# Kernel optimization log

Measured on AMD Instinct MI355X. Metric: run time of the kernel, lower is better.

Reference implementation:

```python
import jax, jax.numpy as jnp
import numpy as np

B, T, D, F0, F1 = 128, 256, 512, 2048, 1024
EPS = 1e-5  # BatchNorm1d eps


def _bn_relu(x, gamma, beta):
    # training-mode BatchNorm1d over the flattened (B*T) batch axis, then ReLU
    mu = x.mean(axis=0)
    var = x.var(axis=0)  # biased variance, as torch BN uses for normalization
    return jax.nn.relu((x - mu) * jax.lax.rsqrt(var + EPS) * gamma + beta)


def _lstm_cell(x, h, c, w_ih, w_hh, b):
    # torch LSTMCell gate order: i, f, g, o
    gates = x @ w_ih.T + h @ w_hh.T + b
    i, f, g, o = jnp.split(gates, 4, axis=-1)
    c = jax.nn.sigmoid(f) * c + jax.nn.sigmoid(i) * jnp.tanh(g)
    h = jax.nn.sigmoid(o) * jnp.tanh(c)
    return h, c


def setup_inputs() -> dict:
    key = jax.random.key(0)
    ks = jax.random.split(key, 24)
    s = 0.02
    inp = {
        "feat0": jax.random.normal(ks[0], (B, T, F0), jnp.float32),
        "feat1": jax.random.normal(ks[1], (B, T, F1), jnp.float32),
        "feat_mask": jnp.ones((B, T), jnp.float32),
        # visual embeddings (Linear + BN affine)
        "w_emb0": jax.random.normal(ks[2], (D, F0), jnp.float32) * s,
        "b_emb0": jnp.zeros((D,), jnp.float32),
        "gamma0": jnp.ones((D,), jnp.float32),
        "beta0": jnp.zeros((D,), jnp.float32),
        "w_emb1": jax.random.normal(ks[3], (D, F1), jnp.float32) * s,
        "b_emb1": jnp.zeros((D,), jnp.float32),
        "gamma1": jnp.ones((D,), jnp.float32),
        "beta1": jnp.zeros((D,), jnp.float32),
        # LSTMCell rgb
        "w_ih0": jax.random.normal(ks[4], (4 * D, D), jnp.float32) * s,
        "w_hh0": jax.random.normal(ks[5], (4 * D, D), jnp.float32) * s,
        "b_ih0": jnp.zeros((4 * D,), jnp.float32),
        "b_hh0": jnp.zeros((4 * D,), jnp.float32),
        # LSTMCell opfl
        "w_ih1": jax.random.normal(ks[6], (4 * D, D), jnp.float32) * s,
        "w_hh1": jax.random.normal(ks[7], (4 * D, D), jnp.float32) * s,
        "b_ih1": jnp.zeros((4 * D,), jnp.float32),
        "b_hh1": jnp.zeros((4 * D,), jnp.float32),
        # Gates: sigmoid(Linear(source)) * target
        "wg0": jax.random.normal(ks[8], (D, D), jnp.float32) * s,
        "bg0": jnp.zeros((D,), jnp.float32),
        "wg1": jax.random.normal(ks[9], (D, D), jnp.float32) * s,
        "bg1": jnp.zeros((D,), jnp.float32),
        # Fusion: tanh(W1 f1 + W2 f2 + b)
        "wf1": jax.random.normal(ks[10], (D, D), jnp.float32) * s,
        "wf2": jax.random.normal(ks[11], (D, D), jnp.float32) * s,
        "bf": jnp.zeros((D,), jnp.float32),
    }
    return inp


def reference(feat0, feat1, feat_mask,
              w_emb0, b_emb0, gamma0, beta0,
              w_emb1, b_emb1, gamma1, beta1,
              w_ih0, w_hh0, b_ih0, b_hh0,
              w_ih1, w_hh1, b_ih1, b_hh1,
              wg0, bg0, wg1, bg1,
              wf1, wf2, bf):
    Bv, Tv = feat0.shape[0], feat0.shape[1]
    # embed + BN(train mode) + ReLU (dropout = identity in eval)
    e0 = _bn_relu(feat0.reshape(-1, feat0.shape[-1]) @ w_emb0.T + b_emb0,
                  gamma0, beta0).reshape(Bv, Tv, -1)
    e1 = _bn_relu(feat1.reshape(-1, feat1.shape[-1]) @ w_emb1.T + b_emb1,
                  gamma1, beta1).reshape(Bv, Tv, -1)

    bc0 = b_ih0 + b_hh0
    bc1 = b_ih1 + b_hh1

    def step(carry, xs):
        h0, c0, h1, c1 = carry
        x0, x1, m = xs  # x: [B, D], m: [B]
        h0, c0 = _lstm_cell(x0, h0, c0, w_ih0, w_hh0, bc0)
        h1, c1 = _lstm_cell(x1, h1, c1, w_ih1, w_hh1, bc1)
        m = m[:, None]
        h0, c0, h1, c1 = h0 * m, c0 * m, h1 * m, c1 * m
        gate0 = jax.nn.sigmoid(h1 @ wg0.T + bg0) * h0  # gate_rgb(h1 -> h0)
        gate1 = jax.nn.sigmoid(h0 @ wg1.T + bg1) * h1  # gate_opfl(h0 -> h1)
        return (h0, c0, h1, c1), (gate0, gate1)

    z = jnp.zeros((Bv, w_hh0.shape[-1]), e0.dtype)
    xs = (e0.transpose(1, 0, 2), e1.transpose(1, 0, 2), feat_mask.T)
    _, (o0, o1) = jax.lax.scan(step, (z, z, z, z), xs)  # [T, B, D]
    o0 = o0.transpose(1, 0, 2)
    o1 = o1.transpose(1, 0, 2)
    # Fusion: tanh(W1 o0 + W2 o1 + b)
    return jnp.tanh(jnp.einsum('btd,ed->bte', o0, wf1)
                    + jnp.einsum('btd,ed->bte', o1, wf2) + bf)
```

## Files before the change

kernel.cpp:

```cpp
#include <hip/hip_runtime.h>
#include <math.h>


typedef short s16x8 __attribute__((ext_vector_type(8)));
typedef float f32x4 __attribute__((ext_vector_type(4)));
typedef float f32x16 __attribute__((ext_vector_type(16)));
typedef unsigned short u16;

__device__ __forceinline__ float sigmoidf_(float x){ return 1.0f/(1.0f+expf(-x)); }

__device__ __forceinline__ u16 f2bf(float x){
  unsigned int u = __float_as_uint(x);
  unsigned int r = u + 0x7fffu + ((u>>16)&1u);
  return (u16)(r>>16);
}
__device__ __forceinline__ float bf2f(u16 s){ return __uint_as_float(((unsigned int)s)<<16); }

__device__ __forceinline__ void unpack8(const unsigned int* __restrict__ p,
                                        s16x8& hi, s16x8& lo){
  uint4 w0 = *(const uint4*)p;
  uint4 w1 = *(const uint4*)(p+4);
  union { unsigned int u[4]; s16x8 v; } H, L;
  H.u[0] = (w0.x>>16) | (w0.y & 0xffff0000u);
  H.u[1] = (w0.z>>16) | (w0.w & 0xffff0000u);
  H.u[2] = (w1.x>>16) | (w1.y & 0xffff0000u);
  H.u[3] = (w1.z>>16) | (w1.w & 0xffff0000u);
  L.u[0] = (w0.x & 0xffffu) | (w0.y<<16);
  L.u[1] = (w0.z & 0xffffu) | (w0.w<<16);
  L.u[2] = (w1.x & 0xffffu) | (w1.y<<16);
  L.u[3] = (w1.z & 0xffffu) | (w1.w<<16);
  hi = H.v; lo = L.v;
}

__global__ __launch_bounds__(256) void split_plain(const float* __restrict__ src,
                                                   u16* __restrict__ hi, u16* __restrict__ lo, int n)
{
  int i = blockIdx.x*256 + threadIdx.x;
  if (i < n){
    float v = src[i];
    u16 h = f2bf(v);
    hi[i] = h;
    lo[i] = f2bf(v - bf2f(h));
  }
}

__global__ __launch_bounds__(256) void split_fragW(const float* __restrict__ src,
                                                   u16* __restrict__ hi, u16* __restrict__ lo,
                                                   int N, int K)
{
  int i = blockIdx.x*256 + threadIdx.x;
  if (i >= N*K) return;
  int n = i / K, k = i - n*K;
  float v = src[i];
  u16 h = f2bf(v), l2 = f2bf(v - bf2f(h));
  size_t off = ((((size_t)(k>>4)*(N/32) + (n>>5))*64) + ((k>>3)&1)*32 + (n&31))*8 + (k&7);
  hi[off] = h; lo[off] = l2;
}

__global__ __launch_bounds__(256) void split_gates2(const float* __restrict__ wih,
                                                    const float* __restrict__ whh,
                                                    const float* __restrict__ bih,
                                                    const float* __restrict__ bhh,
                                                    u16* __restrict__ hi, u16* __restrict__ lo,
                                                    float* __restrict__ bc)
{
  int np = blockIdx.x;
  int d = np>>2, q = np&3;
  int orow = q*512 + d;
  for (int k = threadIdx.x; k < 1024; k += 256){
    float v = (k < 512) ? wih[(size_t)orow*512 + k] : whh[(size_t)orow*512 + (k-512)];
    u16 h = f2bf(v), l2 = f2bf(v - bf2f(h));
    size_t off = (((size_t)(k>>4)*64 + (np>>5))*64 + ((k>>3)&1)*32 + (np&31))*8 + (k&7);
    hi[off] = h; lo[off] = l2;
  }
  if (threadIdx.x == 0) bc[np] = bih[orow] + bhh[orow];
}

__global__ __launch_bounds__(256) void gemm_emb(
    const float* __restrict__ A, const u16* __restrict__ Whi, const u16* __restrict__ Wlo,
    const float* __restrict__ bias, float* __restrict__ out, int K)
{
  __shared__ u16 Ah[128][40];
  __shared__ u16 Al[128][40];
  __shared__ u16 Wh[128][40];
  __shared__ u16 Wl[128][40];

  int bx = blockIdx.x;
  int nt = bx & 3, mt = bx >> 2;
  int m0 = mt*128, n0 = nt*128;
  int tid = threadIdx.x, lane = tid & 63, w = tid >> 6;
  int wm = (w>>1)*64, wn = (w&1)*64;

  f32x4 acc[4][4];
  #pragma unroll
  for (int i=0;i<4;i++)
    #pragma unroll
    for (int j=0;j<4;j++) acc[i][j] = (f32x4){0.f,0.f,0.f,0.f};

  for (int k0=0; k0<K; k0+=32){
    #pragma unroll
    for (int p=0;p<4;p++){
      int fi = p*256 + tid;
      int r = fi>>3, c = fi&7;
      float4 v = *(const float4*)&A[(size_t)(m0+r)*K + k0 + c*4];
      u16 h0=f2bf(v.x), h1=f2bf(v.y), h2=f2bf(v.z), h3=f2bf(v.w);
      u16 l0=f2bf(v.x-bf2f(h0)), l1=f2bf(v.y-bf2f(h1)), l2=f2bf(v.z-bf2f(h2)), l3=f2bf(v.w-bf2f(h3));
      uint2 ph = { (unsigned)h0 | ((unsigned)h1<<16), (unsigned)h2 | ((unsigned)h3<<16) };
      uint2 pl = { (unsigned)l0 | ((unsigned)l1<<16), (unsigned)l2 | ((unsigned)l3<<16) };
      *(uint2*)&Ah[r][c*4] = ph;
      *(uint2*)&Al[r][c*4] = pl;
    }
    #pragma unroll
    for (int p=0;p<2;p++){
      int fi = p*256 + tid;
      int r = fi>>2, c = fi&3;
      uint4 vh = *(const uint4*)&Whi[(size_t)(n0+r)*K + k0 + c*8];
      uint4 vl = *(const uint4*)&Wlo[(size_t)(n0+r)*K + k0 + c*8];
      *(uint4*)&Wh[r][c*8] = vh;
      *(uint4*)&Wl[r][c*8] = vl;
    }
    __syncthreads();
    s16x8 ah[4], al[4];
    #pragma unroll
    for (int mf=0;mf<4;mf++){
      ah[mf] = *(const s16x8*)&Ah[wm + mf*16 + (lane&15)][(lane>>4)*8];
      al[mf] = *(const s16x8*)&Al[wm + mf*16 + (lane&15)][(lane>>4)*8];
    }
    #pragma unroll
    for (int nf=0;nf<4;nf++){
      s16x8 wh = *(const s16x8*)&Wh[wn + nf*16 + (lane&15)][(lane>>4)*8];
      s16x8 wl = *(const s16x8*)&Wl[wn + nf*16 + (lane&15)][(lane>>4)*8];
      #pragma unroll
      for (int mf=0;mf<4;mf++){
        acc[mf][nf] = __builtin_amdgcn_mfma_f32_16x16x32_bf16(ah[mf], wh, acc[mf][nf], 0,0,0);
        acc[mf][nf] = __builtin_amdgcn_mfma_f32_16x16x32_bf16(ah[mf], wl, acc[mf][nf], 0,0,0);
        acc[mf][nf] = __builtin_amdgcn_mfma_f32_16x16x32_bf16(al[mf], wh, acc[mf][nf], 0,0,0);
      }
    }
    __syncthreads();
  }
  #pragma unroll
  for (int mf=0;mf<4;mf++){
    #pragma unroll
    for (int nf=0;nf<4;nf++){
      int col = n0 + wn + nf*16 + (lane&15);
      int row0 = m0 + wm + mf*16 + (lane>>4)*4;
      float b = bias[col];
      #pragma unroll
      for (int g=0; g<4; ++g){
        out[(size_t)(row0+g)*512 + col] = acc[mf][nf][g] + b;
      }
    }
  }
}

__global__ __launch_bounds__(256) void bn_stats1(const float* __restrict__ Y,
                                                 float* __restrict__ psum,
                                                 float* __restrict__ psq)
{
  int blk = blockIdx.x;
  int tid = threadIdx.x;
  const float* base = Y + (size_t)blk*256*512;
  float sx=0.f, sy=0.f, qx=0.f, qy=0.f;
  for (int r=0;r<256;r++){
    float2 v = *(const float2*)&base[(size_t)r*512 + tid*2];
    sx += v.x; sy += v.y; qx += v.x*v.x; qy += v.y*v.y;
  }
  psum[(size_t)blk*512 + tid*2]   = sx;
  psum[(size_t)blk*512 + tid*2+1] = sy;
  psq [(size_t)blk*512 + tid*2]   = qx;
  psq [(size_t)blk*512 + tid*2+1] = qy;
}

__global__ __launch_bounds__(512) void bn_stats2(const float* __restrict__ psum,
                                                 const float* __restrict__ psq,
                                                 float* __restrict__ mean,
                                                 float* __restrict__ scale)
{
  int c = threadIdx.x;
  float s=0.f, q=0.f;
  for (int b=0;b<128;b++){ s += psum[(size_t)b*512+c]; q += psq[(size_t)b*512+c]; }
  float mu = s * (1.0f/32768.0f);
  float var = q * (1.0f/32768.0f) - mu*mu;
  mean[c] = mu;
  scale[c] = rsqrtf(var + 1e-5f);
}

__global__ __launch_bounds__(256) void bn_apply_split(const float* __restrict__ Y,
                                                      const float* __restrict__ mean,
                                                      const float* __restrict__ scale,
                                                      const float* __restrict__ gamma,
                                                      const float* __restrict__ beta,
                                                      u16* __restrict__ ehi, u16* __restrict__ elo)
{
  size_t idx = (size_t)blockIdx.x*256 + threadIdx.x;
  int r = (int)(idx >> 6);
  int c0 = (int)(idx & 63) * 8;
  int b = r >> 8, t = r & 255;
  float4 v0 = *(const float4*)&Y[(size_t)r*512 + c0];
  float4 v1 = *(const float4*)&Y[(size_t)r*512 + c0 + 4];
  float vv[8] = {v0.x,v0.y,v0.z,v0.w,v1.x,v1.y,v1.z,v1.w};
  unsigned int hw[4], lw[4];
  #pragma unroll
  for (int u=0;u<8;u+=2){
    float xa = fmaxf((vv[u]  -mean[c0+u])  *scale[c0+u]  *gamma[c0+u]  +beta[c0+u],   0.f);
    float xb = fmaxf((vv[u+1]-mean[c0+u+1])*scale[c0+u+1]*gamma[c0+u+1]+beta[c0+u+1], 0.f);
    u16 ha = f2bf(xa), hb = f2bf(xb);
    u16 la = f2bf(xa - bf2f(ha)), lb = f2bf(xb - bf2f(hb));
    hw[u>>1] = (unsigned)ha | ((unsigned)hb<<16);
    lw[u>>1] = (unsigned)la | ((unsigned)lb<<16);
  }
  size_t off = (size_t)t*65536 + ((((size_t)(c0>>4)*4 + (b>>5))*64) + ((c0>>3)&1)*32 + (b&31))*8;
  uint4 ph = {hw[0],hw[1],hw[2],hw[3]};
  uint4 pl = {lw[0],lw[1],lw[2],lw[3]};
  *(uint4*)&ehi[off] = ph;
  *(uint4*)&elo[off] = pl;
}

__global__ __launch_bounds__(256) void zero_init(int* __restrict__ bar,
                                                 unsigned* __restrict__ H0,
                                                 unsigned* __restrict__ H1)
{
  int i = blockIdx.x*256 + threadIdx.x;
  if (i < 6144) bar[i] = 0;
  H0[i] = 0u;
  H1[i] = 0u;
}

struct ScanArgs {
  const u16 *e0hi, *e0lo, *e1hi, *e1lo;
  const u16 *wr0hi, *wr0lo, *wr1hi, *wr1lo;
  const float *bc0, *bc1, *mask;
  unsigned *H0, *H1;
  int *flags;
  int *gen;
};

__global__ __launch_bounds__(256) void scan_all(ScanArgs A)
{
  __shared__ u16 Wlds[64][64][8];
  __shared__ float red[2][2][16][65];
  __shared__ int sig;
  __shared__ int fcnt;

  int bx = blockIdx.x;
  int ci = bx>>7, s = (bx>>1)&63, rh = bx&1;
  int dom = ci*2 + rh;
  int cb = s;
  int tid = threadIdx.x, lane = tid&63, w = tid>>6;
  int khalf = w>>1, pr = w&1;
  int rt = rh*2 + pr;
  bool mast = (cb == 0);

  int* flags = A.flags + dom*64*16;
  int* gen   = A.gen   + dom*32*16;

  const u16* ehi = ci? A.e1hi : A.e0hi;
  const u16* elo = ci? A.e1lo : A.e0lo;
  const u16* whi = ci? A.wr1hi : A.wr0hi;
  const u16* wlo = ci? A.wr1lo : A.wr0lo;
  const float* bc = ci? A.bc1 : A.bc0;
  unsigned* Hc = ci? A.H1 : A.H0;

  if (tid == 0){ sig = 0; fcnt = 0; }

  for (int it=0; it<16; ++it){
    int cid = it*256 + tid;
    int ks = cid>>6, l8 = cid&63;
    const u16* src = whi + (((size_t)ks*64 + s)*64 + l8)*8;
    *(uint4*)&Wlds[ks][l8][0] = *(const uint4*)src;
  }
  __syncthreads();

  int q = lane&3;
  int np = s*32 + (lane&31);
  int d  = np>>2;
  float bcv = bc[np];
  float creg[4] = {0.f,0.f,0.f,0.f};

  for (int t=0; t<256; ++t){
    size_t abase = (size_t)t*65536;

    if (khalf == 0){
      f32x16 a0=(f32x16)(0.f), a1=(f32x16)(0.f), a2=(f32x16)(0.f);
      #pragma unroll 4
      for (int kk=0; kk<32; ++kk){
        size_t aoff = abase + ((size_t)(kk*4 + rt)*64 + lane)*8;
        s16x8 fah = *(const s16x8*)(ehi + aoff);
        s16x8 fal = *(const s16x8*)(elo + aoff);
        s16x8 fwh = *(const s16x8*)&Wlds[kk][lane][0];
        s16x8 fwl = *(const s16x8*)(wlo + (((size_t)kk*64 + s)*64 + lane)*8);
        a0 = __builtin_amdgcn_mfma_f32_32x32x16_bf16(fah, fwh, a0, 0,0,0);
        a1 = __builtin_amdgcn_mfma_f32_32x32x16_bf16(fah, fwl, a1, 0,0,0);
        a2 = __builtin_amdgcn_mfma_f32_32x32x16_bf16(fal, fwh, a2, 0,0,0);
      }
      f32x16 t3 = a0 + a1 + a2;
      #pragma unroll
      for (int e=0;e<16;e++) red[t&1][pr][e][lane] = t3[e];
      __syncthreads();
    } else {
      if (lane == 0){
        while (__hip_atomic_load(&gen[(cb&31)*16], __ATOMIC_RELAXED, __HIP_MEMORY_SCOPE_AGENT) < t)
          __builtin_amdgcn_s_sleep(1);
      }
      asm volatile("" ::: "memory");

      f32x16 a0=(f32x16)(0.f), a1=(f32x16)(0.f), a2=(f32x16)(0.f);
      #pragma unroll 8
      for (int kk=0; kk<32; ++kk){
        size_t aoff = abase + ((size_t)(kk*4 + rt)*64 + lane)*8;
        s16x8 fah, fal;
        unpack8(Hc + aoff, fah, fal);
        int ks = 32 + kk;
        s16x8 fwh = *(const s16x8*)&Wlds[ks][lane][0];
        s16x8 fwl = *(const s16x8*)(wlo + (((size_t)ks*64 + s)*64 + lane)*8);
        a0 = __builtin_amdgcn_mfma_f32_32x32x16_bf16(fah, fwh, a0, 0,0,0);
        a1 = __builtin_amdgcn_mfma_f32_32x32x16_bf16(fah, fwl, a1, 0,0,0);
        a2 = __builtin_amdgcn_mfma_f32_32x32x16_bf16(fal, fwh, a2, 0,0,0);
      }
      f32x16 mine = a0 + a1 + a2;
      __syncthreads();

      f32x16 tot;
      #pragma unroll
      for (int e=0;e<16;e++) tot[e] = mine[e] + red[t&1][pr][e][lane];

      size_t hSlot = (size_t)(t+1)*65536;
      #pragma unroll
      for (int r=0;r<16;r++){
        float pre = tot[r] + bcv;
        float act = (q==2) ? tanhf(pre) : sigmoidf_(pre);
        float v1 = __shfl_xor(act, 1);
        float v2 = __shfl_xor(act, 2);
        float v3 = __shfl_xor(v1, 2);
        float gi = (q==0)? act : (q==1)? v1 : (q==2)? v2 : v3;
        float gf = (q==1)? act : (q==0)? v1 : (q==3)? v2 : v3;
        float gg = (q==2)? act : (q==3)? v1 : (q==0)? v2 : v3;
        float go = (q==3)? act : (q==2)? v1 : (q==1)? v2 : v3;
        if (q == (r&3)){
          int ri = r>>2;
          int row = rh*64 + pr*32 + (r&3) + 8*ri + 4*(lane>>5);
          float cold = creg[ri];
          float cn = gf*cold + gi*gg;
          float h  = go*tanhf(cn);
          float mv = A.mask[(size_t)row*256 + t];
          cn *= mv; h *= mv;
          creg[ri] = cn;
          u16 hh = f2bf(h), hl = f2bf(h - bf2f(hh));
          size_t hoff = hSlot + ((((size_t)(d>>4)*4 + (row>>5))*64) + ((d>>3)&1)*32 + (row&31))*8 + (d&7);
          atomicExch(&Hc[hoff], ((unsigned)hh<<16) | (unsigned)hl);
        }
      }
      asm volatile("s_waitcnt vmcnt(0)" ::: "memory");
      if (lane == 0) atomicAdd(&sig, 1);

      if (mast){
        int fi = tid - 128;
        if (fi >= 1 && fi < 64){
          while (__hip_atomic_load(&flags[fi*16], __ATOMIC_RELAXED, __HIP_MEMORY_SCOPE_AGENT) < t+1)
            __builtin_amdgcn_s_sleep(1);
          atomicAdd(&fcnt, 1);
        }
        if (tid == 128){
          while (__hip_atomic_load(&sig, __ATOMIC_RELAXED, __HIP_MEMORY_SCOPE_WORKGROUP) < 2*(t+1))
            __builtin_amdgcn_s_sleep(1);
          while (__hip_atomic_load(&fcnt, __ATOMIC_RELAXED, __HIP_MEMORY_SCOPE_WORKGROUP) < 63*(t+1))
            __builtin_amdgcn_s_sleep(1);
        }
        if (w == 2 && lane < 32){
          atomicExch(&gen[lane*16], t+1);
        }
      } else {
        if (tid == 128){
          while (__hip_atomic_load(&sig, __ATOMIC_RELAXED, __HIP_MEMORY_SCOPE_WORKGROUP) < 2*(t+1))
            __builtin_amdgcn_s_sleep(1);
          atomicExch(&flags[cb*16], t+1);
        }
      }
    }
  }
}

__global__ __launch_bounds__(256,1) void gemm_gate(
    const unsigned* __restrict__ Aint,
    const u16* __restrict__ Whi,  const u16* __restrict__ Wlo,
    const float* __restrict__ bias,
    const unsigned* __restrict__ OtInt,
    u16* __restrict__ outHi, u16* __restrict__ outLo)
{
  int bx = blockIdx.x;
  int nt = bx & 7, mt = bx >> 3;
  int n0 = nt*64;
  int tid = threadIdx.x, lane = tid & 63, w = tid >> 6;
  size_t aBase = (size_t)mt*65536;

  f32x16 a0[2], a1[2], a2[2];
  #pragma unroll
  for (int c=0;c<2;c++){
    a0[c]=(f32x16)(0.f); a1[c]=(f32x16)(0.f); a2[c]=(f32x16)(0.f);
  }

  #pragma unroll 2
  for (int kk=0; kk<32; ++kk){
    size_t aoff = aBase + (((size_t)kk*4 + w)*64 + lane)*8;
    s16x8 fah, fal;
    unpack8(Aint + aoff, fah, fal);
    #pragma unroll
    for (int c=0;c<2;c++){
      size_t woff = (((size_t)kk*16 + nt*2 + c)*64 + lane)*8;
      s16x8 fwh = *(const s16x8*)(Whi + woff);
      s16x8 fwl = *(const s16x8*)(Wlo + woff);
      a0[c] = __builtin_amdgcn_mfma_f32_32x32x16_bf16(fah, fwh, a0[c], 0,0,0);
      a1[c] = __builtin_amdgcn_mfma_f32_32x32x16_bf16(fah, fwl, a1[c], 0,0,0);
      a2[c] = __builtin_amdgcn_mfma_f32_32x32x16_bf16(fal, fwh, a2[c], 0,0,0);
    }
  }

  #pragma unroll
  for (int c=0;c<2;c++){
    f32x16 acc = a0[c] + a1[c] + a2[c];
    int col = n0 + c*32 + (lane&31);
    float b = bias[col];
    #pragma unroll
    for (int r=0;r<16;r++){
      int row = w*32 + (r&3) + 8*(r>>2) + 4*(lane>>5);
      float v = acc[r] + b;
      size_t foff = aBase + ((((size_t)(col>>4)*4 + w)*64) + ((col>>3)&1)*32 + (row&31))*8 + (col&7);
      unsigned ov = OtInt[foff];
      float other = bf2f((u16)(ov>>16)) + bf2f((u16)(ov&0xffffu));
      v = sigmoidf_(v) * other;
      u16 hh = f2bf(v);
      u16 hl = f2bf(v - bf2f(hh));
      outHi[foff] = hh;
      outLo[foff] = hl;
    }
  }
}

__global__ __launch_bounds__(256,1) void gemm_final(
    const u16* __restrict__ Ahi,  const u16* __restrict__ Alo,
    const u16* __restrict__ A2hi, const u16* __restrict__ A2lo,
    const u16* __restrict__ Whi,  const u16* __restrict__ Wlo,
    const u16* __restrict__ W2hi, const u16* __restrict__ W2lo,
    const float* __restrict__ bias,
    float* __restrict__ outF)
{
  int bx = blockIdx.x;
  int nt = bx & 7, mt = bx >> 3;
  int n0 = nt*64;
  int tid = threadIdx.x, lane = tid & 63, w = tid >> 6;
  size_t aBase = (size_t)mt*65536;

  f32x16 a0[2], a1[2], a2[2];
  #pragma unroll
  for (int c=0;c<2;c++){
    a0[c]=(f32x16)(0.f); a1[c]=(f32x16)(0.f); a2[c]=(f32x16)(0.f);
  }

  for (int pair=0; pair<2; ++pair){
    const u16* ah = pair ? A2hi : Ahi;
    const u16* al = pair ? A2lo : Alo;
    const u16* wh = pair ? W2hi : Whi;
    const u16* wl = pair ? W2lo : Wlo;
    #pragma unroll 2
    for (int kk=0; kk<32; ++kk){
      size_t aoff = aBase + (((size_t)kk*4 + w)*64 + lane)*8;
      s16x8 fah = *(const s16x8*)(ah + aoff);
      s16x8 fal = *(const s16x8*)(al + aoff);
      #pragma unroll
      for (int c=0;c<2;c++){
        size_t woff = (((size_t)kk*16 + nt*2 + c)*64 + lane)*8;
        s16x8 fwh = *(const s16x8*)(wh + woff);
        s16x8 fwl = *(const s16x8*)(wl + woff);
        a0[c] = __builtin_amdgcn_mfma_f32_32x32x16_bf16(fah, fwh, a0[c], 0,0,0);
        a1[c] = __builtin_amdgcn_mfma_f32_32x32x16_bf16(fah, fwl, a1[c], 0,0,0);
        a2[c] = __builtin_amdgcn_mfma_f32_32x32x16_bf16(fal, fwh, a2[c], 0,0,0);
      }
    }
  }

  #pragma unroll
  for (int c=0;c<2;c++){
    f32x16 acc = a0[c] + a1[c] + a2[c];
    int col = n0 + c*32 + (lane&31);
    float b = bias[col];
    #pragma unroll
    for (int r=0;r<16;r++){
      int row = w*32 + (r&3) + 8*(r>>2) + 4*(lane>>5);
      float v = tanhf(acc[r] + b);
      outF[((size_t)row*256 + mt)*512 + col] = v;
    }
  }
}

extern "C" void kernel_launch(void* const* d_in, const int* in_sizes, int n_in,
                              void* d_out, int out_size, void* d_ws, size_t ws_size,
                              hipStream_t stream)
{
  const float* feat0  = (const float*)d_in[0];
  const float* feat1  = (const float*)d_in[1];
  const float* fmask  = (const float*)d_in[2];
  const float* w_emb0 = (const float*)d_in[3];
  const float* b_emb0 = (const float*)d_in[4];
  const float* gamma0 = (const float*)d_in[5];
  const float* beta0  = (const float*)d_in[6];
  const float* w_emb1 = (const float*)d_in[7];
  const float* b_emb1 = (const float*)d_in[8];
  const float* gamma1 = (const float*)d_in[9];
  const float* beta1  = (const float*)d_in[10];
  const float* w_ih0  = (const float*)d_in[11];
  const float* w_hh0  = (const float*)d_in[12];
  const float* b_ih0  = (const float*)d_in[13];
  const float* b_hh0  = (const float*)d_in[14];
  const float* w_ih1  = (const float*)d_in[15];
  const float* w_hh1  = (const float*)d_in[16];
  const float* b_ih1  = (const float*)d_in[17];
  const float* b_hh1  = (const float*)d_in[18];
  const float* wg0    = (const float*)d_in[19];
  const float* bg0    = (const float*)d_in[20];
  const float* wg1    = (const float*)d_in[21];
  const float* bg1    = (const float*)d_in[22];
  const float* wf1    = (const float*)d_in[23];
  const float* wf2    = (const float*)d_in[24];
  const float* bf     = (const float*)d_in[25];
  float* out = (float*)d_out;

  char* ws = (char*)d_ws;
  u16* e0hi = (u16*)(ws + 0);
  u16* e0lo = (u16*)(ws + 33554432);
  u16* e1hi = (u16*)(ws + 67108864);
  u16* e1lo = (u16*)(ws + 100663296);
  unsigned* H0int = (unsigned*)(ws + 134217728);
  unsigned* H1int = (unsigned*)(ws + 201588736);
  int*   barp  = (int*)(ws + 269484032);
  float* psum  = (float*)(ws + 269484032);
  float* psq   = (float*)(ws + 269746176);
  float* meanb = (float*)(ws + 270008320);
  float* scaleb= (float*)(ws + 270010368);
  float* bc0   = (float*)(ws + 270012416);
  float* bc1   = (float*)(ws + 270020608);
  u16* wr0hi = (u16*)(ws + 270028800);
  u16* wr0lo = (u16*)(ws + 274223104);
  u16* wr1hi = (u16*)(ws + 278417408);
  u16* wr1lo = (u16*)(ws + 282611712);
  u16* we0hi = (u16*)(ws + 286806016);
  u16* we0lo = (u16*)(ws + 288903168);
  u16* we1hi = (u16*)(ws + 291000320);
  u16* we1lo = (u16*)(ws + 292048896);
  u16* wg0hi = (u16*)(ws + 293097472);
  u16* wg0lo = (u16*)(ws + 293621760);
  u16* wg1hi = (u16*)(ws + 294146048);
  u16* wg1lo = (u16*)(ws + 294670336);
  u16* wf1hi = (u16*)(ws + 295194624);
  u16* wf1lo = (u16*)(ws + 295718912);
  u16* wf2hi = (u16*)(ws + 296243200);
  u16* wf2lo = (u16*)(ws + 296767488);
  float* Ytmp = (float*)(ws + 134217728);

  split_gates2<<<dim3(2048), dim3(256), 0, stream>>>(w_ih0, w_hh0, b_ih0, b_hh0, wr0hi, wr0lo, bc0);
  split_gates2<<<dim3(2048), dim3(256), 0, stream>>>(w_ih1, w_hh1, b_ih1, b_hh1, wr1hi, wr1lo, bc1);
  split_plain<<<dim3(4096), dim3(256), 0, stream>>>(w_emb0, we0hi, we0lo, 1048576);
  split_plain<<<dim3(2048), dim3(256), 0, stream>>>(w_emb1, we1hi, we1lo, 524288);
  split_fragW<<<dim3(1024), dim3(256), 0, stream>>>(wg0, wg0hi, wg0lo, 512, 512);
  split_fragW<<<dim3(1024), dim3(256), 0, stream>>>(wg1, wg1hi, wg1lo, 512, 512);
  split_fragW<<<dim3(1024), dim3(256), 0, stream>>>(wf1, wf1hi, wf1lo, 512, 512);
  split_fragW<<<dim3(1024), dim3(256), 0, stream>>>(wf2, wf2hi, wf2lo, 512, 512);

  gemm_emb<<<dim3(1024), dim3(256), 0, stream>>>(feat0, we0hi, we0lo, b_emb0, Ytmp, 2048);
  bn_stats1<<<dim3(128), dim3(256), 0, stream>>>(Ytmp, psum, psq);
  bn_stats2<<<dim3(1),   dim3(512), 0, stream>>>(psum, psq, meanb, scaleb);
  bn_apply_split<<<dim3(8192), dim3(256), 0, stream>>>(Ytmp, meanb, scaleb, gamma0, beta0, e0hi, e0lo);

  gemm_emb<<<dim3(1024), dim3(256), 0, stream>>>(feat1, we1hi, we1lo, b_emb1, Ytmp, 1024);
  bn_stats1<<<dim3(128), dim3(256), 0, stream>>>(Ytmp, psum, psq);
  bn_stats2<<<dim3(1),   dim3(512), 0, stream>>>(psum, psq, meanb, scaleb);
  bn_apply_split<<<dim3(8192), dim3(256), 0, stream>>>(Ytmp, meanb, scaleb, gamma1, beta1, e1hi, e1lo);

  zero_init<<<dim3(256), dim3(256), 0, stream>>>(barp, H0int, H1int);
  ScanArgs sa;
  sa.e0hi=e0hi; sa.e0lo=e0lo; sa.e1hi=e1hi; sa.e1lo=e1lo;
  sa.wr0hi=wr0hi; sa.wr0lo=wr0lo; sa.wr1hi=wr1hi; sa.wr1lo=wr1lo;
  sa.bc0=bc0; sa.bc1=bc1; sa.mask=fmask;
  sa.H0=H0int; sa.H1=H1int;
  sa.flags=barp; sa.gen=barp + 4*64*16;
  scan_all<<<dim3(256), dim3(256), 0, stream>>>(sa);

  gemm_gate<<<dim3(2048), dim3(256), 0, stream>>>(
      H1int + 65536, wg0hi, wg0lo, bg0, H0int + 65536, e0hi, e0lo);
  gemm_gate<<<dim3(2048), dim3(256), 0, stream>>>(
      H0int + 65536, wg1hi, wg1lo, bg1, H1int + 65536, e1hi, e1lo);
  gemm_final<<<dim3(2048), dim3(256), 0, stream>>>(
      e0hi, e0lo, e1hi, e1lo,
      wf1hi, wf1lo, wf2hi, wf2lo, bf, out);
}
```

Measured before the change: 7.485 ms.

## Replace master-gathered generation barrier with direct all-flag polling in scan

The per-timestep grid barrier in the recurrent scan kernel changes from a two-level scheme, where a master block gathers 63 flags and then broadcasts a generation counter, to a flat scheme. Every block's 64 lanes now poll all 64 per-block flags in their domain. This removes one serial hop (gather plus broadcast) from the critical path of each of the 256 timesteps. In exchange it adds more polling traffic on the flag cache lines, since every block reads every flag.

Result: no change. 7.532 ms (+0.6%).

```diff
diff --git a/kernel.cpp b/kernel.cpp
--- a/kernel.cpp
+++ b/kernel.cpp
@@ -222,7 +222,7 @@
                                                  unsigned* __restrict__ H1)
 {
   int i = blockIdx.x*256 + threadIdx.x;
-  if (i < 6144) bar[i] = 0;
+  if (i < 4096) bar[i] = 0;
   H0[i] = 0u;
   H1[i] = 0u;
 }
@@ -233,7 +233,6 @@
   const float *bc0, *bc1, *mask;
   unsigned *H0, *H1;
   int *flags;
-  int *gen;
 };
 
 __global__ __launch_bounds__(256) void scan_all(ScanArgs A)
@@ -241,7 +240,6 @@
   __shared__ u16 Wlds[64][64][8];
   __shared__ float red[2][2][16][65];
   __shared__ int sig;
-  __shared__ int fcnt;
 
   int bx = blockIdx.x;
   int ci = bx>>7, s = (bx>>1)&63, rh = bx&1;
@@ -250,10 +248,8 @@
   int tid = threadIdx.x, lane = tid&63, w = tid>>6;
   int khalf = w>>1, pr = w&1;
   int rt = rh*2 + pr;
-  bool mast = (cb == 0);
 
   int* flags = A.flags + dom*64*16;
-  int* gen   = A.gen   + dom*32*16;
 
   const u16* ehi = ci? A.e1hi : A.e0hi;
   const u16* elo = ci? A.e1lo : A.e0lo;
@@ -262,7 +258,7 @@
   const float* bc = ci? A.bc1 : A.bc0;
   unsigned* Hc = ci? A.H1 : A.H0;
 
-  if (tid == 0){ sig = 0; fcnt = 0; }
+  if (tid == 0) sig = 0;
 
   for (int it=0; it<16; ++it){
     int cid = it*256 + tid;
@@ -299,9 +295,12 @@
       for (int e=0;e<16;e++) red[t&1][pr][e][lane] = t3[e];
       __syncthreads();
     } else {
-      if (lane == 0){
-        while (__hip_atomic_load(&gen[(cb&31)*16], __ATOMIC_RELAXED, __HIP_MEMORY_SCOPE_AGENT) < t)
-          __builtin_amdgcn_s_sleep(1);
+      {
+        int v;
+        do {
+          v = __hip_atomic_load(&flags[lane*16], __ATOMIC_RELAXED, __HIP_MEMORY_SCOPE_AGENT);
+          if (v < t) __builtin_amdgcn_s_sleep(1);
+        } while (v < t);
       }
       asm volatile("" ::: "memory");
 
@@ -353,29 +352,10 @@
       }
       asm volatile("s_waitcnt vmcnt(0)" ::: "memory");
       if (lane == 0) atomicAdd(&sig, 1);
-
-      if (mast){
-        int fi = tid - 128;
-        if (fi >= 1 && fi < 64){
-          while (__hip_atomic_load(&flags[fi*16], __ATOMIC_RELAXED, __HIP_MEMORY_SCOPE_AGENT) < t+1)
-            __builtin_amdgcn_s_sleep(1);
-          atomicAdd(&fcnt, 1);
-        }
-        if (tid == 128){
-          while (__hip_atomic_load(&sig, __ATOMIC_RELAXED, __HIP_MEMORY_SCOPE_WORKGROUP) < 2*(t+1))
-            __builtin_amdgcn_s_sleep(1);
-          while (__hip_atomic_load(&fcnt, __ATOMIC_RELAXED, __HIP_MEMORY_SCOPE_WORKGROUP) < 63*(t+1))
-            __builtin_amdgcn_s_sleep(1);
-        }
-        if (w == 2 && lane < 32){
-          atomicExch(&gen[lane*16], t+1);
-        }
-      } else {
-        if (tid == 128){
-          while (__hip_atomic_load(&sig, __ATOMIC_RELAXED, __HIP_MEMORY_SCOPE_WORKGROUP) < 2*(t+1))
-            __builtin_amdgcn_s_sleep(1);
-          atomicExch(&flags[cb*16], t+1);
-        }
+      if (tid == 128){
+        while (__hip_atomic_load(&sig, __ATOMIC_RELAXED, __HIP_MEMORY_SCOPE_WORKGROUP) < 2*(t+1))
+          __builtin_amdgcn_s_sleep(1);
+        atomicExch(&flags[cb*16], t+1);
       }
     }
   }
@@ -582,7 +562,7 @@
   sa.wr0hi=wr0hi; sa.wr0lo=wr0lo; sa.wr1hi=wr1hi; sa.wr1lo=wr1lo;
   sa.bc0=bc0; sa.bc1=bc1; sa.mask=fmask;
   sa.H0=H0int; sa.H1=H1int;
-  sa.flags=barp; sa.gen=barp + 4*64*16;
+  sa.flags=barp;
   scan_all<<<dim3(256), dim3(256), 0, stream>>>(sa);
 
   gemm_gate<<<dim3(2048), dim3(256), 0, stream>>>(
```
